# Performance work log

Hardware: AMD Instinct MI355X
Metric: run time of the kernel (lower is better)

## Reference

```python
import jax, jax.numpy as jnp
import numpy as np

N_HEAD, D_K, D_V, D_MODEL = 12, 64, 64, 768
SMOOTH = 1e-06
LN_EPS = 1e-06


def _layer_norm(x, g, b, eps=LN_EPS):
    m = x.mean(-1, keepdims=True)
    v = x.var(-1, keepdims=True)
    return (x - m) / jnp.sqrt(v + eps) * g + b


def setup_inputs() -> dict:
    key = jax.random.key(0)
    ks = jax.random.split(key, 12)
    b, L, R = 4, 1024, 97
    w = lambda k, i, o: jax.random.normal(k, (i, o), jnp.float32) * 0.02
    return {
        'doc_input': jax.random.normal(ks[0], (b, L, D_MODEL), jnp.float32),
        'rel_input': jax.random.normal(ks[1], (b, R, D_MODEL), jnp.float32),
        'mask': jax.random.randint(ks[2], (b, L), 0, 2, jnp.int32),
        'wq_doc': w(ks[3], D_MODEL, N_HEAD * D_K),
        'wk_doc': w(ks[4], D_MODEL, N_HEAD * D_K),
        'wv_doc': w(ks[5], D_MODEL, N_HEAD * D_V),
        'wk_rel': w(ks[6], D_MODEL, N_HEAD * D_K),
        'wv_rel': w(ks[7], D_MODEL, N_HEAD * D_V),
        'fc_doc': w(ks[8], N_HEAD * D_V, D_MODEL),
        'fc_rel': w(ks[9], N_HEAD * D_V, D_MODEL),
        'ln_doc_g': jnp.ones((D_MODEL,), jnp.float32),
        'ln_doc_b': jnp.zeros((D_MODEL,), jnp.float32),
        'ln_rel_g': jnp.ones((D_MODEL,), jnp.float32),
        'ln_rel_b': jnp.zeros((D_MODEL,), jnp.float32),
    }


def _forward(doc_input, rel_input, mask, wq_doc, wk_doc, wv_doc, wk_rel, wv_rel,
             fc_doc, fc_rel, ln_doc_g, ln_doc_b, ln_rel_g, ln_rel_b):
    b, L, _ = doc_input.shape
    R = rel_input.shape[1]
    proj = lambda x, w, d: (x @ w).reshape(x.shape[0], x.shape[1], N_HEAD, d).transpose(0, 2, 1, 3)
    dq = proj(doc_input, wq_doc, D_K)   # [b,h,L,dk]
    dk = proj(doc_input, wk_doc, D_K)
    dv = proj(doc_input, wv_doc, D_V)
    rk = proj(rel_input, wk_rel, D_K)   # [b,h,R,dk]
    rv = proj(rel_input, wv_rel, D_V)

    scale = 1.0 / np.sqrt(D_K).astype(np.float32)
    key_mask = (mask == 0)[:, None, None, :]  # [b,1,1,L]

    # doc-doc attention with relation-summed key fusion
    fused_k = dk + rk.sum(2, keepdims=True)  # broadcast [b,h,1,dk]
    scores = jnp.einsum('bhid,bhjd->bhij', dq, fused_k) * scale + SMOOTH
    scores = jnp.where(key_mask, -1e9, scores)
    alpha_dd = jax.nn.softmax(scores, axis=-1)  # dropout disabled (eval)

    # per-relation cross attention, batched over R (replaces python loop)
    rscores = jnp.einsum('bhrd,bhjd->bhrj', rk, dk) * scale + SMOOTH
    rscores = jnp.where(key_mask, -1e9, rscores)
    alpha_r = jax.nn.softmax(rscores, axis=-1)
    psi_r = jnp.einsum('bhrj,bhjd->bhrd', alpha_r, dv) + rv  # [b,h,R,dv]
    psi_r = psi_r.transpose(0, 2, 1, 3).reshape(b, R, N_HEAD * D_V)
    rel_output = _layer_norm(psi_r @ fc_rel + rel_input, ln_rel_g, ln_rel_b)

    fused_v = dv + rv.sum(2, keepdims=True)
    psi_i = jnp.einsum('bhij,bhjd->bhid', alpha_dd, fused_v)  # [b,h,L,dv]
    psi_i = psi_i.transpose(0, 2, 1, 3).reshape(b, L, N_HEAD * D_V)
    doc_output = _layer_norm(psi_i @ fc_doc + doc_input, ln_doc_g, ln_doc_b)
    return doc_output, rel_output


def reference(doc_input, rel_input, mask, wq_doc, wk_doc, wv_doc, wk_rel, wv_rel,
              fc_doc, fc_rel, ln_doc_g, ln_doc_b, ln_rel_g, ln_rel_b):
    return _forward(doc_input, rel_input, mask, wq_doc, wk_doc, wv_doc, wk_rel,
                    wv_rel, fc_doc, fc_rel, ln_doc_g, ln_doc_b, ln_rel_g, ln_rel_b)
```

## Files before the change

kernel.cpp:

```cpp
#include <hip/hip_runtime.h>

typedef __attribute__((ext_vector_type(8))) short bt8;
typedef __attribute__((ext_vector_type(4))) float f32x4;

__device__ __forceinline__ float bf2f(ushort u) {
    union { unsigned int i; float f; } v; v.i = ((unsigned int)u) << 16; return v.f;
}
__device__ __forceinline__ ushort f2bf(float f) {
    union { float f; unsigned int i; } v; v.f = f;
    unsigned int r = v.i + 0x7fffu + ((v.i >> 16) & 1u);
    return (ushort)(r >> 16);
}

#define GLOAD_LDS16(gp, lp) __builtin_amdgcn_global_load_lds( \
    (const __attribute__((address_space(1))) unsigned int*)(gp), \
    (__attribute__((address_space(3))) unsigned int*)(lp), 16, 0, 0)

__global__ __launch_bounds__(256) void cvt_bf16(const float* __restrict__ in,
                                                ushort* __restrict__ out, int n) {
    int i = blockIdx.x * 256 + threadIdx.x;
    if (i < n) out[i] = f2bf(in[i]);
}

__global__ void transpose_all(const float* __restrict__ p0, const float* __restrict__ p1,
                              const float* __restrict__ p2, const float* __restrict__ p3,
                              const float* __restrict__ p4, const float* __restrict__ p5,
                              const float* __restrict__ p6, ushort* __restrict__ out) {
    __shared__ float t[32][33];
    const float* W;
    switch (blockIdx.z) {
        case 0: W = p0; break; case 1: W = p1; break; case 2: W = p2; break;
        case 3: W = p3; break; case 4: W = p4; break; case 5: W = p5; break;
        default: W = p6; break;
    }
    ushort* WT = out + (size_t)blockIdx.z * 768 * 768;
    int bx = blockIdx.x * 32, by = blockIdx.y * 32;
    int x = threadIdx.x, y0 = threadIdx.y;
    for (int y = y0; y < 32; y += 8)
        t[y][x] = W[(size_t)(by + y) * 768 + bx + x];
    __syncthreads();
    for (int y = y0; y < 32; y += 8)
        WT[(size_t)(bx + y) * 768 + by + x] = f2bf(t[x][y]);
}

template<bool BF16O>
__global__ __launch_bounds__(256) void gemm_gl(
    const ushort* __restrict__ A, const ushort* __restrict__ BT,
    void* __restrict__ Cv, int M, int N, int K)
{
    __shared__ ushort As[128 * 32];
    __shared__ ushort Bs[128 * 32];
    const int tid = threadIdx.x;
    const int wave = tid >> 6, lane = tid & 63;
    const int row0 = blockIdx.x * 128, col0 = blockIdx.y * 128;
    const int wm = (wave >> 1) * 64, wn = (wave & 1) * 64;
    const int lr = lane & 15, lk = (lane >> 4) * 8;
    const int srow = wave * 16 + (lane >> 2);
    const int scol = (lane & 3) * 8;

    f32x4 acc[4][4];
    #pragma unroll
    for (int mi = 0; mi < 4; ++mi)
        #pragma unroll
        for (int ni = 0; ni < 4; ++ni)
            acc[mi][ni] = (f32x4){0.f, 0.f, 0.f, 0.f};

    int ar0 = row0 + srow;       if (ar0 >= M) ar0 = M - 1;
    int ar1 = row0 + 64 + srow;  if (ar1 >= M) ar1 = M - 1;
    const int bc0 = col0 + srow, bc1 = col0 + 64 + srow;

    for (int kt = 0; kt < K; kt += 32) {
        __syncthreads();
        GLOAD_LDS16(A + (size_t)ar0 * K + kt + scol, As + wave * 512);
        GLOAD_LDS16(A + (size_t)ar1 * K + kt + scol, As + 2048 + wave * 512);
        GLOAD_LDS16(BT + (size_t)bc0 * K + kt + scol, Bs + wave * 512);
        GLOAD_LDS16(BT + (size_t)bc1 * K + kt + scol, Bs + 2048 + wave * 512);
        __syncthreads();
        bt8 af[4], bf[4];
        #pragma unroll
        for (int mi = 0; mi < 4; ++mi)
            af[mi] = *(const bt8*)&As[(wm + mi * 16 + lr) * 32 + lk];
        #pragma unroll
        for (int ni = 0; ni < 4; ++ni)
            bf[ni] = *(const bt8*)&Bs[(wn + ni * 16 + lr) * 32 + lk];
        #pragma unroll
        for (int mi = 0; mi < 4; ++mi)
            #pragma unroll
            for (int ni = 0; ni < 4; ++ni)
                acc[mi][ni] = __builtin_amdgcn_mfma_f32_16x16x32_bf16(
                    af[mi], bf[ni], acc[mi][ni], 0, 0, 0);
    }

    #pragma unroll
    for (int mi = 0; mi < 4; ++mi) {
        int orow0 = row0 + wm + mi * 16 + (lane >> 4) * 4;
        #pragma unroll
        for (int ni = 0; ni < 4; ++ni) {
            int ocol = col0 + wn + ni * 16 + lr;
            if (ocol >= N) continue;
            #pragma unroll
            for (int r2 = 0; r2 < 4; ++r2) {
                int orow = orow0 + r2;
                if (orow < M) {
                    if (BF16O)
                        ((ushort*)Cv)[(size_t)orow * N + ocol] = f2bf(acc[mi][ni][r2]);
                    else
                        ((float*)Cv)[(size_t)orow * N + ocol] = acc[mi][ni][r2];
                }
            }
        }
    }
}

__global__ void relsum(const ushort* __restrict__ rkv,
                       float* __restrict__ rks, float* __restrict__ rvs) {
    int b = blockIdx.x;
    int c = blockIdx.y * 256 + threadIdx.x;
    float s1 = 0.f, s2 = 0.f;
    for (int r = 0; r < 97; ++r) {
        const ushort* row = rkv + (size_t)(b * 97 + r) * 1536;
        s1 += bf2f(row[c]);
        s2 += bf2f(row[768 + c]);
    }
    rks[b * 768 + c] = s1;
    rvs[b * 768 + c] = s2;
}

__global__ __launch_bounds__(256) void fusekv(
    const ushort* __restrict__ qkv, const float* __restrict__ rks,
    const float* __restrict__ rvs, ushort* __restrict__ kf, ushort* __restrict__ vf)
{
    int row = blockIdx.x;
    int c = blockIdx.y * 256 + threadIdx.x;
    int b = row >> 10;
    size_t qi = (size_t)row * 2304;
    size_t oi = (size_t)row * 768 + c;
    kf[oi] = f2bf(bf2f(qkv[qi + 768 + c]) + rks[b * 768 + c]);
    vf[oi] = f2bf(bf2f(qkv[qi + 1536 + c]) + rvs[b * 768 + c]);
}

__global__ __launch_bounds__(256) void attn_mfma(
    const ushort* __restrict__ Qp, int qstride, size_t qbstride, int qmax,
    const ushort* __restrict__ Kp, const ushort* __restrict__ Vp,
    int kvstride, size_t kvbstride,
    const int* __restrict__ mask,
    float* __restrict__ Mo, float* __restrict__ Lo, ushort* __restrict__ Oo,
    int nspl, int ntiles, int qrows)
{
    __shared__ ushort Ks[64 * 64];
    __shared__ ushort Vt[64 * 64];
    __shared__ ushort Ps[4][16 * 64];
    __shared__ float  madd[64];

    const int tid = threadIdx.x;
    const int wv = tid >> 6, lane = tid & 63;
    const int lr = lane & 15, lk = (lane >> 4) * 8, rg = lane >> 4;
    const int bh = blockIdx.x, b = bh / 12, h = bh % 12;
    const int qb = blockIdx.y, spl = blockIdx.z;
    const int q0 = qb * 64 + wv * 16;

    const size_t kvbase = (size_t)b * kvbstride + h * 64;
    const size_t qbase  = (size_t)b * qbstride + h * 64;

    bt8 qf[2];
    {
        const int qi = q0 + lr;
        if (qi < qmax) {
            const ushort* qp = Qp + qbase + (size_t)qi * qstride + lk;
            qf[0] = *(const bt8*)qp;
            qf[1] = *(const bt8*)(qp + 32);
        } else {
            #pragma unroll
            for (int j = 0; j < 8; ++j) { qf[0][j] = 0; qf[1][j] = 0; }
        }
    }

    f32x4 acc[4];
    #pragma unroll
    for (int dg = 0; dg < 4; ++dg) acc[dg] = (f32x4){0.f, 0.f, 0.f, 0.f};
    float m_r[4], l_r[4];
    #pragma unroll
    for (int r = 0; r < 4; ++r) { m_r[r] = -3.0e38f; l_r[r] = 0.f; }

    const int key = tid >> 2, c0 = (tid & 3) * 16;
    const int vd = tid & 63, vw = tid >> 6;
    const int swk = (key & 7) << 3;
    const int swv = (vd & 7) << 3;
    const int swl = (lr & 7) << 3;

    for (int t = 0; t < ntiles; ++t) {
        const int k0 = (spl * ntiles + t) * 64;
        __syncthreads();
        {
            const ushort* src = Kp + kvbase + (size_t)(k0 + key) * kvstride + c0;
            int4 a = *(const int4*)src;
            int4 bq = *(const int4*)(src + 8);
            *(int4*)&Ks[key * 64 + (c0 ^ swk)] = a;
            *(int4*)&Ks[key * 64 + ((c0 + 8) ^ swk)] = bq;
        }
        {
            const ushort* vsrc = Vp + kvbase + (size_t)(k0 + vw * 16) * kvstride + vd;
            ushort tv[16];
            #pragma unroll
            for (int j = 0; j < 16; ++j) tv[j] = vsrc[(size_t)j * kvstride];
            const int cc = vw * 16;
            *(int4*)&Vt[vd * 64 + (cc ^ swv)] = *(int4*)tv;
            *(int4*)&Vt[vd * 64 + ((cc + 8) ^ swv)] = *(int4*)(tv + 8);
        }
        if (tid < 64)
            madd[tid] = (mask[b * 1024 + k0 + tid] == 0) ? -1e30f : 0.f;
        __syncthreads();

        f32x4 sf[4];
        #pragma unroll
        for (int kg = 0; kg < 4; ++kg) {
            f32x4 s4 = (f32x4){0.f, 0.f, 0.f, 0.f};
            #pragma unroll
            for (int kk = 0; kk < 2; ++kk) {
                bt8 kf2 = *(const bt8*)&Ks[(kg * 16 + lr) * 64 + ((kk * 32 + lk) ^ swl)];
                s4 = __builtin_amdgcn_mfma_f32_16x16x32_bf16(qf[kk], kf2, s4, 0, 0, 0);
            }
            sf[kg] = s4;
        }

        float pv[4][4];
        #pragma unroll
        for (int r = 0; r < 4; ++r) {
            float sv0 = sf[0][r] * 0.125f + madd[lr];
            float sv1 = sf[1][r] * 0.125f + madd[16 + lr];
            float sv2 = sf[2][r] * 0.125f + madd[32 + lr];
            float sv3 = sf[3][r] * 0.125f + madd[48 + lr];
            float mx = fmaxf(fmaxf(sv0, sv1), fmaxf(sv2, sv3));
            mx = fmaxf(mx, __shfl_xor(mx, 1));
            mx = fmaxf(mx, __shfl_xor(mx, 2));
            mx = fmaxf(mx, __shfl_xor(mx, 4));
            mx = fmaxf(mx, __shfl_xor(mx, 8));
            float mn = fmaxf(m_r[r], mx);
            float corr = __expf(m_r[r] - mn);
            m_r[r] = mn;
            float p0 = __expf(sv0 - mn), p1 = __expf(sv1 - mn);
            float p2 = __expf(sv2 - mn), p3 = __expf(sv3 - mn);
            pv[0][r] = p0; pv[1][r] = p1; pv[2][r] = p2; pv[3][r] = p3;
            float ps = (p0 + p1) + (p2 + p3);
            ps += __shfl_xor(ps, 1);
            ps += __shfl_xor(ps, 2);
            ps += __shfl_xor(ps, 4);
            ps += __shfl_xor(ps, 8);
            l_r[r] = l_r[r] * corr + ps;
            #pragma unroll
            for (int dg = 0; dg < 4; ++dg) acc[dg][r] *= corr;
        }

        #pragma unroll
        for (int kg = 0; kg < 4; ++kg)
            #pragma unroll
            for (int r = 0; r < 4; ++r) {
                int rowq = rg * 4 + r;
                Ps[wv][rowq * 64 + ((kg * 16 + lr) ^ ((rowq & 7) << 3))] = f2bf(pv[kg][r]);
            }

        #pragma unroll
        for (int kk = 0; kk < 2; ++kk) {
            bt8 pa = *(const bt8*)&Ps[wv][lr * 64 + ((kk * 32 + lk) ^ swl)];
            #pragma unroll
            for (int dg = 0; dg < 4; ++dg) {
                bt8 vf2 = *(const bt8*)&Vt[(dg * 16 + lr) * 64 + ((kk * 32 + lk) ^ swl)];
                acc[dg] = __builtin_amdgcn_mfma_f32_16x16x32_bf16(pa, vf2, acc[dg], 0, 0, 0);
            }
        }
    }

    if (lr == 0) {
        #pragma unroll
        for (int r = 0; r < 4; ++r) {
            int qi = q0 + rg * 4 + r;
            int prow = (bh * nspl + spl) * qrows + qi;
            Mo[prow] = m_r[r];
            Lo[prow] = l_r[r];
        }
    }
    #pragma unroll
    for (int r = 0; r < 4; ++r) {
        int qi = q0 + rg * 4 + r;
        size_t orow = ((size_t)(bh * nspl + spl) * qrows + qi) * 64;
        #pragma unroll
        for (int dg = 0; dg < 4; ++dg)
            Oo[orow + dg * 16 + lr] = f2bf(acc[dg][r]);
    }
}

__global__ __launch_bounds__(64) void attn_merge(
    const float* __restrict__ Mo, const float* __restrict__ Lo, const ushort* __restrict__ Oo,
    const ushort* __restrict__ resid, size_t rbstride, int rstride,
    ushort* __restrict__ psi,
    int nspl, int qrows, int qmax, int out_rows)
{
    const int tid = threadIdx.x, bh = blockIdx.x, qb = blockIdx.y;
    const int b = bh / 12, h = bh % 12;
    const int qi = qb * 64 + tid;
    if (qi >= qmax) return;
    const int pb = bh * nspl;

    float M = -3.0e38f;
    for (int s = 0; s < nspl; ++s)
        M = fmaxf(M, Mo[(pb + s) * qrows + qi]);
    float L = 0.f, O[64];
    #pragma unroll
    for (int d = 0; d < 64; ++d) O[d] = 0.f;
    for (int s = 0; s < nspl; ++s) {
        int pr = (pb + s) * qrows + qi;
        float f = __expf(Mo[pr] - M);
        L += Lo[pr] * f;
        const uint* op = (const uint*)(Oo + (size_t)pr * 64);
        #pragma unroll
        for (int d2 = 0; d2 < 32; ++d2) {
            uint u = op[d2];
            O[2*d2]   += f * bf2f((ushort)(u & 0xffffu));
            O[2*d2+1] += f * bf2f((ushort)(u >> 16));
        }
    }
    const float rl = 1.f / L;
    const size_t ob = ((size_t)b * out_rows + qi) * 768 + h * 64;
    if (resid) {
        const ushort* rp = resid + (size_t)b * rbstride + (size_t)qi * rstride + h * 64;
        #pragma unroll
        for (int d = 0; d < 64; ++d)
            psi[ob + d] = f2bf(O[d] * rl + bf2f(rp[d]));
    } else {
        #pragma unroll
        for (int d = 0; d < 64; ++d)
            psi[ob + d] = f2bf(O[d] * rl);
    }
}

__global__ __launch_bounds__(256) void ln_ker(
    const float* __restrict__ gin, const float* __restrict__ resid,
    const float* __restrict__ g, const float* __restrict__ bta,
    float* __restrict__ out)
{
    const int row = blockIdx.x, tid = threadIdx.x;
    const size_t rb = (size_t)row * 768;
    float x[3], s = 0.f, s2 = 0.f;
    #pragma unroll
    for (int k2 = 0; k2 < 3; ++k2) {
        int c = k2 * 256 + tid;
        float v = gin[rb + c] + resid[rb + c];
        x[k2] = v; s += v; s2 += v * v;
    }
    #pragma unroll
    for (int off = 32; off > 0; off >>= 1) {
        s  += __shfl_down(s, off);
        s2 += __shfl_down(s2, off);
    }
    __shared__ float red[10];
    const int wv = tid >> 6;
    if ((tid & 63) == 0) { red[wv] = s; red[4 + wv] = s2; }
    __syncthreads();
    if (tid == 0) {
        float ts = red[0] + red[1] + red[2] + red[3];
        float t2 = red[4] + red[5] + red[6] + red[7];
        float mean = ts * (1.f / 768.f);
        float var = t2 * (1.f / 768.f) - mean * mean;
        red[8] = mean;
        red[9] = rsqrtf(fmaxf(var, 0.f) + 1e-6f);
    }
    __syncthreads();
    const float mean = red[8], rstd = red[9];
    #pragma unroll
    for (int k2 = 0; k2 < 3; ++k2) {
        int c = k2 * 256 + tid;
        out[rb + c] = (x[k2] - mean) * rstd * g[c] + bta[c];
    }
}

extern "C" void kernel_launch(void* const* d_in, const int* in_sizes, int n_in,
                              void* d_out, int out_size, void* d_ws, size_t ws_size,
                              hipStream_t stream) {
    const float* doc  = (const float*)d_in[0];
    const float* rel  = (const float*)d_in[1];
    const int*   mask = (const int*)d_in[2];
    const float* ln_dg = (const float*)d_in[10];
    const float* ln_db = (const float*)d_in[11];
    const float* ln_rg = (const float*)d_in[12];
    const float* ln_rb = (const float*)d_in[13];

    char* ws = (char*)d_ws;
    size_t off = 0;
    ushort* wtall = (ushort*)(ws + off); off += (size_t)7 * 768 * 768 * 2;
    ushort* wtqkv = wtall;
    ushort* wt34  = wtall + (size_t)3 * 768 * 768;
    ushort* wt5   = wtall + (size_t)5 * 768 * 768;
    ushort* wt6   = wtall + (size_t)6 * 768 * 768;
    ushort* doc_bf = (ushort*)(ws + off); off += (size_t)4096 * 768 * 2;
    ushort* rel_bf = (ushort*)(ws + off); off += (size_t)388 * 768 * 2;
    ushort* qkv_bf = (ushort*)(ws + off); off += (size_t)4096 * 2304 * 2;
    ushort* rkv_bf = (ushort*)(ws + off); off += (size_t)388 * 1536 * 2;
    float*  rks = (float*)(ws + off); off += (size_t)4 * 768 * 4;
    float*  rvs = (float*)(ws + off); off += (size_t)4 * 768 * 4;
    ushort* kf_bf = (ushort*)(ws + off); off += (size_t)4096 * 768 * 2;
    ushort* vf_bf = (ushort*)(ws + off); off += (size_t)4096 * 768 * 2;
    ushort* psi_i = (ushort*)(ws + off); off += (size_t)4096 * 768 * 2;
    ushort* psi_r = (ushort*)(ws + off); off += (size_t)388 * 768 * 2;
    float*  Mo = (float*)(ws + off);  off += (size_t)48 * 2 * 1024 * 4;
    float*  Lo = (float*)(ws + off);  off += (size_t)48 * 2 * 1024 * 4;
    ushort* Oo = (ushort*)(ws + off); off += (size_t)48 * 2 * 1024 * 64 * 2;
    float*  gdoc = (float*)(ws + off); off += (size_t)4096 * 768 * 4;
    float*  grel = (float*)(ws + off); off += (size_t)388 * 768 * 4;

    float* out_doc = (float*)d_out;
    float* out_rel = out_doc + (size_t)4096 * 768;

    cvt_bf16<<<dim3((4096 * 768 + 255) / 256), 256, 0, stream>>>(doc, doc_bf, 4096 * 768);
    cvt_bf16<<<dim3((388 * 768 + 255) / 256), 256, 0, stream>>>(rel, rel_bf, 388 * 768);
    transpose_all<<<dim3(24, 24, 7), dim3(32, 8), 0, stream>>>(
        (const float*)d_in[3], (const float*)d_in[4], (const float*)d_in[5],
        (const float*)d_in[6], (const float*)d_in[7], (const float*)d_in[8],
        (const float*)d_in[9], wtall);

    gemm_gl<true><<<dim3(32, 18), 256, 0, stream>>>(doc_bf, wtqkv, qkv_bf, 4096, 2304, 768);
    gemm_gl<true><<<dim3(4, 12),  256, 0, stream>>>(rel_bf, wt34, rkv_bf, 388, 1536, 768);

    relsum<<<dim3(4, 3), 256, 0, stream>>>(rkv_bf, rks, rvs);
    fusekv<<<dim3(4096, 3), 256, 0, stream>>>(qkv_bf, rks, rvs, kf_bf, vf_bf);

    attn_mfma<<<dim3(48, 2, 8), 256, 0, stream>>>(
        rkv_bf, 1536, (size_t)97 * 1536, 97,
        qkv_bf + 768, qkv_bf + 1536, 2304, (size_t)1024 * 2304,
        mask, Mo, Lo, Oo, 8, 2, 128);
    attn_merge<<<dim3(48, 2), 64, 0, stream>>>(
        Mo, Lo, Oo, rkv_bf + 768, (size_t)97 * 1536, 1536, psi_r, 8, 128, 97, 97);

    attn_mfma<<<dim3(48, 16, 2), 256, 0, stream>>>(
        qkv_bf, 2304, (size_t)1024 * 2304, 1024,
        kf_bf, vf_bf, 768, (size_t)1024 * 768,
        mask, Mo, Lo, Oo, 2, 8, 1024);
    attn_merge<<<dim3(48, 16), 64, 0, stream>>>(
        Mo, Lo, Oo, (const ushort*)nullptr, 0, 0, psi_i, 2, 1024, 1024, 1024);

    gemm_gl<false><<<dim3(32, 6), 256, 0, stream>>>(psi_i, wt5, gdoc, 4096, 768, 768);
    gemm_gl<false><<<dim3(4, 6),  256, 0, stream>>>(psi_r, wt6, grel, 388, 768, 768);

    ln_ker<<<4096, 256, 0, stream>>>(gdoc, doc, ln_dg, ln_db, out_doc);
    ln_ker<<<388,  256, 0, stream>>>(grel, rel, ln_rg, ln_rb, out_rel);
}
```

Measured before the change: 216.3 us.

## Widen attention query tile, add lazy-rescale exp2 softmax, small-tile GEMMs, fused convert

The attention kernel now gives each wave 32 query rows instead of 16, so each block covers 128 queries and the K/V tiles loaded into shared memory are reused across twice as many rows. The softmax switches to exp2 with the scale folded into one constant, and it rescales the running max only when the max grows by more than a threshold. A new 64x64-tile GEMM replaces the larger-tile GEMM for the small and output projections to launch more blocks. The two fp32-to-bf16 conversions are merged into one launch. The costs are more registers per thread in attention and possible numeric drift from the deferred rescale.

```diff
diff --git a/kernel.cpp b/kernel.cpp
--- a/kernel.cpp
+++ b/kernel.cpp
@@ -16,10 +16,12 @@
     (const __attribute__((address_space(1))) unsigned int*)(gp), \
     (__attribute__((address_space(3))) unsigned int*)(lp), 16, 0, 0)
 
-__global__ __launch_bounds__(256) void cvt_bf16(const float* __restrict__ in,
-                                                ushort* __restrict__ out, int n) {
+__global__ __launch_bounds__(256) void cvt_two(
+    const float* __restrict__ a, const float* __restrict__ b,
+    ushort* __restrict__ oa, ushort* __restrict__ ob, int n1, int n2) {
     int i = blockIdx.x * 256 + threadIdx.x;
-    if (i < n) out[i] = f2bf(in[i]);
+    if (i < n1) oa[i] = f2bf(a[i]);
+    else if (i < n1 + n2) ob[i - n1] = f2bf(b[i - n1]);
 }
 
 __global__ void transpose_all(const float* __restrict__ p0, const float* __restrict__ p1,
@@ -112,6 +114,72 @@
     }
 }
 
+template<bool BF16O>
+__global__ __launch_bounds__(256) void gemm64(
+    const ushort* __restrict__ A, const ushort* __restrict__ BT,
+    void* __restrict__ Cv, int M, int N, int K)
+{
+    __shared__ ushort As[64 * 32];
+    __shared__ ushort Bs[64 * 32];
+    const int tid = threadIdx.x;
+    const int wave = tid >> 6, lane = tid & 63;
+    const int row0 = blockIdx.x * 64, col0 = blockIdx.y * 64;
+    const int wm = (wave >> 1) * 32, wn = (wave & 1) * 32;
+    const int lr = lane & 15, lk = (lane >> 4) * 8;
+    const int srow = tid >> 2;
+    const int scol = (tid & 3) * 8;
+
+    f32x4 acc[2][2];
+    #pragma unroll
+    for (int mi = 0; mi < 2; ++mi)
+        #pragma unroll
+        for (int ni = 0; ni < 2; ++ni)
+            acc[mi][ni] = (f32x4){0.f, 0.f, 0.f, 0.f};
+
+    int ar = row0 + srow; if (ar >= M) ar = M - 1;
+    const int bc = col0 + srow;
+
+    for (int kt = 0; kt < K; kt += 32) {
+        __syncthreads();
+        GLOAD_LDS16(A + (size_t)ar * K + kt + scol, As + wave * 512);
+        GLOAD_LDS16(BT + (size_t)bc * K + kt + scol, Bs + wave * 512);
+        __syncthreads();
+        bt8 af[2], bf[2];
+        #pragma unroll
+        for (int mi = 0; mi < 2; ++mi)
+            af[mi] = *(const bt8*)&As[(wm + mi * 16 + lr) * 32 + lk];
+        #pragma unroll
+        for (int ni = 0; ni < 2; ++ni)
+            bf[ni] = *(const bt8*)&Bs[(wn + ni * 16 + lr) * 32 + lk];
+        #pragma unroll
+        for (int mi = 0; mi < 2; ++mi)
+            #pragma unroll
+            for (int ni = 0; ni < 2; ++ni)
+                acc[mi][ni] = __builtin_amdgcn_mfma_f32_16x16x32_bf16(
+                    af[mi], bf[ni], acc[mi][ni], 0, 0, 0);
+    }
+
+    #pragma unroll
+    for (int mi = 0; mi < 2; ++mi) {
+        int orow0 = row0 + wm + mi * 16 + (lane >> 4) * 4;
+        #pragma unroll
+        for (int ni = 0; ni < 2; ++ni) {
+            int ocol = col0 + wn + ni * 16 + lr;
+            if (ocol >= N) continue;
+            #pragma unroll
+            for (int r2 = 0; r2 < 4; ++r2) {
+                int orow = orow0 + r2;
+                if (orow < M) {
+                    if (BF16O)
+                        ((ushort*)Cv)[(size_t)orow * N + ocol] = f2bf(acc[mi][ni][r2]);
+                    else
+                        ((float*)Cv)[(size_t)orow * N + ocol] = acc[mi][ni][r2];
+                }
+            }
+        }
+    }
+}
+
 __global__ void relsum(const ushort* __restrict__ rkv,
                        float* __restrict__ rks, float* __restrict__ rvs) {
     int b = blockIdx.x;
@@ -139,6 +207,9 @@
     vf[oi] = f2bf(bf2f(qkv[qi + 1536 + c]) + rvs[b * 768 + c]);
 }
 
+#define SC2 0.18033688011112042f
+#define THR2 10.0f
+
 __global__ __launch_bounds__(256) void attn_mfma(
     const ushort* __restrict__ Qp, int qstride, size_t qbstride, int qmax,
     const ushort* __restrict__ Kp, const ushort* __restrict__ Vp,
@@ -149,7 +220,7 @@
 {
     __shared__ ushort Ks[64 * 64];
     __shared__ ushort Vt[64 * 64];
-    __shared__ ushort Ps[4][16 * 64];
+    __shared__ ushort Ps[4][32 * 64];
     __shared__ float  madd[64];
 
     const int tid = threadIdx.x;
@@ -157,30 +228,33 @@
     const int lr = lane & 15, lk = (lane >> 4) * 8, rg = lane >> 4;
     const int bh = blockIdx.x, b = bh / 12, h = bh % 12;
     const int qb = blockIdx.y, spl = blockIdx.z;
-    const int q0 = qb * 64 + wv * 16;
+    const int q0 = qb * 128 + wv * 32;
 
     const size_t kvbase = (size_t)b * kvbstride + h * 64;
     const size_t qbase  = (size_t)b * qbstride + h * 64;
 
-    bt8 qf[2];
-    {
-        const int qi = q0 + lr;
+    bt8 qf[2][2];
+    #pragma unroll
+    for (int qh = 0; qh < 2; ++qh) {
+        const int qi = q0 + qh * 16 + lr;
         if (qi < qmax) {
             const ushort* qp = Qp + qbase + (size_t)qi * qstride + lk;
-            qf[0] = *(const bt8*)qp;
-            qf[1] = *(const bt8*)(qp + 32);
+            qf[qh][0] = *(const bt8*)qp;
+            qf[qh][1] = *(const bt8*)(qp + 32);
         } else {
             #pragma unroll
-            for (int j = 0; j < 8; ++j) { qf[0][j] = 0; qf[1][j] = 0; }
-        }
-    }
-
-    f32x4 acc[4];
-    #pragma unroll
-    for (int dg = 0; dg < 4; ++dg) acc[dg] = (f32x4){0.f, 0.f, 0.f, 0.f};
-    float m_r[4], l_r[4];
-    #pragma unroll
-    for (int r = 0; r < 4; ++r) { m_r[r] = -3.0e38f; l_r[r] = 0.f; }
+            for (int j = 0; j < 8; ++j) { qf[qh][0][j] = 0; qf[qh][1][j] = 0; }
+        }
+    }
+
+    f32x4 acc[2][4];
+    #pragma unroll
+    for (int qh = 0; qh < 2; ++qh)
+        #pragma unroll
+        for (int dg = 0; dg < 4; ++dg) acc[qh][dg] = (f32x4){0.f, 0.f, 0.f, 0.f};
+    float m_r[8], l_r[8];
+    #pragma unroll
+    for (int r = 0; r < 8; ++r) { m_r[r] = -3.0e38f; l_r[r] = 0.f; }
 
     const int key = tid >> 2, c0 = (tid & 3) * 16;
     const int vd = tid & 63, vw = tid >> 6;
@@ -211,82 +285,93 @@
             madd[tid] = (mask[b * 1024 + k0 + tid] == 0) ? -1e30f : 0.f;
         __syncthreads();
 
-        f32x4 sf[4];
-        #pragma unroll
-        for (int kg = 0; kg < 4; ++kg) {
-            f32x4 s4 = (f32x4){0.f, 0.f, 0.f, 0.f};
+        #pragma unroll
+        for (int qh = 0; qh < 2; ++qh) {
+            f32x4 sf[4];
+            #pragma unroll
+            for (int kg = 0; kg < 4; ++kg) {
+                f32x4 s4 = (f32x4){0.f, 0.f, 0.f, 0.f};
+                #pragma unroll
+                for (int kk = 0; kk < 2; ++kk) {
+                    bt8 kf2 = *(const bt8*)&Ks[(kg * 16 + lr) * 64 + ((kk * 32 + lk) ^ swl)];
+                    s4 = __builtin_amdgcn_mfma_f32_16x16x32_bf16(qf[qh][kk], kf2, s4, 0, 0, 0);
+                }
+                sf[kg] = s4;
+            }
+
+            #pragma unroll
+            for (int r = 0; r < 4; ++r) {
+                const int ri = qh * 4 + r;
+                float sv0 = sf[0][r] * SC2 + madd[lr];
+                float sv1 = sf[1][r] * SC2 + madd[16 + lr];
+                float sv2 = sf[2][r] * SC2 + madd[32 + lr];
+                float sv3 = sf[3][r] * SC2 + madd[48 + lr];
+                float mx = fmaxf(fmaxf(sv0, sv1), fmaxf(sv2, sv3));
+                mx = fmaxf(mx, __shfl_xor(mx, 1));
+                mx = fmaxf(mx, __shfl_xor(mx, 2));
+                mx = fmaxf(mx, __shfl_xor(mx, 4));
+                mx = fmaxf(mx, __shfl_xor(mx, 8));
+                float m_old = m_r[ri];
+                if (mx > m_old + THR2) {
+                    float corr = exp2f(m_old - mx);
+                    m_r[ri] = mx;
+                    l_r[ri] *= corr;
+                    #pragma unroll
+                    for (int dg = 0; dg < 4; ++dg) acc[qh][dg][r] *= corr;
+                }
+                const float mn = m_r[ri];
+                float p0 = exp2f(sv0 - mn), p1 = exp2f(sv1 - mn);
+                float p2 = exp2f(sv2 - mn), p3 = exp2f(sv3 - mn);
+                float ps = (p0 + p1) + (p2 + p3);
+                ps += __shfl_xor(ps, 1);
+                ps += __shfl_xor(ps, 2);
+                ps += __shfl_xor(ps, 4);
+                ps += __shfl_xor(ps, 8);
+                l_r[ri] += ps;
+                const int rowq = qh * 16 + rg * 4 + r;
+                const int swp = (rowq & 7) << 3;
+                Ps[wv][rowq * 64 + ((0 * 16 + lr) ^ swp)] = f2bf(p0);
+                Ps[wv][rowq * 64 + ((1 * 16 + lr) ^ swp)] = f2bf(p1);
+                Ps[wv][rowq * 64 + ((2 * 16 + lr) ^ swp)] = f2bf(p2);
+                Ps[wv][rowq * 64 + ((3 * 16 + lr) ^ swp)] = f2bf(p3);
+            }
+        }
+
+        #pragma unroll
+        for (int qh = 0; qh < 2; ++qh) {
             #pragma unroll
             for (int kk = 0; kk < 2; ++kk) {
-                bt8 kf2 = *(const bt8*)&Ks[(kg * 16 + lr) * 64 + ((kk * 32 + lk) ^ swl)];
-                s4 = __builtin_amdgcn_mfma_f32_16x16x32_bf16(qf[kk], kf2, s4, 0, 0, 0);
+                bt8 pa = *(const bt8*)&Ps[wv][(qh * 16 + lr) * 64 + ((kk * 32 + lk) ^ swl)];
+                #pragma unroll
+                for (int dg = 0; dg < 4; ++dg) {
+                    bt8 vf2 = *(const bt8*)&Vt[(dg * 16 + lr) * 64 + ((kk * 32 + lk) ^ swl)];
+                    acc[qh][dg] = __builtin_amdgcn_mfma_f32_16x16x32_bf16(pa, vf2, acc[qh][dg], 0, 0, 0);
+                }
             }
-            sf[kg] = s4;
-        }
-
-        float pv[4][4];
+        }
+    }
+
+    if (lr == 0) {
+        #pragma unroll
+        for (int qh = 0; qh < 2; ++qh)
+            #pragma unroll
+            for (int r = 0; r < 4; ++r) {
+                int qi = q0 + qh * 16 + rg * 4 + r;
+                int prow = (bh * nspl + spl) * qrows + qi;
+                Mo[prow] = m_r[qh * 4 + r];
+                Lo[prow] = l_r[qh * 4 + r];
+            }
+    }
+    #pragma unroll
+    for (int qh = 0; qh < 2; ++qh)
         #pragma unroll
         for (int r = 0; r < 4; ++r) {
-            float sv0 = sf[0][r] * 0.125f + madd[lr];
-            float sv1 = sf[1][r] * 0.125f + madd[16 + lr];
-            float sv2 = sf[2][r] * 0.125f + madd[32 + lr];
-            float sv3 = sf[3][r] * 0.125f + madd[48 + lr];
-            float mx = fmaxf(fmaxf(sv0, sv1), fmaxf(sv2, sv3));
-            mx = fmaxf(mx, __shfl_xor(mx, 1));
-            mx = fmaxf(mx, __shfl_xor(mx, 2));
-            mx = fmaxf(mx, __shfl_xor(mx, 4));
-            mx = fmaxf(mx, __shfl_xor(mx, 8));
-            float mn = fmaxf(m_r[r], mx);
-            float corr = __expf(m_r[r] - mn);
-            m_r[r] = mn;
-            float p0 = __expf(sv0 - mn), p1 = __expf(sv1 - mn);
-            float p2 = __expf(sv2 - mn), p3 = __expf(sv3 - mn);
-            pv[0][r] = p0; pv[1][r] = p1; pv[2][r] = p2; pv[3][r] = p3;
-            float ps = (p0 + p1) + (p2 + p3);
-            ps += __shfl_xor(ps, 1);
-            ps += __shfl_xor(ps, 2);
-            ps += __shfl_xor(ps, 4);
-            ps += __shfl_xor(ps, 8);
-            l_r[r] = l_r[r] * corr + ps;
-            #pragma unroll
-            for (int dg = 0; dg < 4; ++dg) acc[dg][r] *= corr;
-        }
-
-        #pragma unroll
-        for (int kg = 0; kg < 4; ++kg)
-            #pragma unroll
-            for (int r = 0; r < 4; ++r) {
-                int rowq = rg * 4 + r;
-                Ps[wv][rowq * 64 + ((kg * 16 + lr) ^ ((rowq & 7) << 3))] = f2bf(pv[kg][r]);
-            }
-
-        #pragma unroll
-        for (int kk = 0; kk < 2; ++kk) {
-            bt8 pa = *(const bt8*)&Ps[wv][lr * 64 + ((kk * 32 + lk) ^ swl)];
-            #pragma unroll
-            for (int dg = 0; dg < 4; ++dg) {
-                bt8 vf2 = *(const bt8*)&Vt[(dg * 16 + lr) * 64 + ((kk * 32 + lk) ^ swl)];
-                acc[dg] = __builtin_amdgcn_mfma_f32_16x16x32_bf16(pa, vf2, acc[dg], 0, 0, 0);
-            }
-        }
-    }
-
-    if (lr == 0) {
-        #pragma unroll
-        for (int r = 0; r < 4; ++r) {
-            int qi = q0 + rg * 4 + r;
-            int prow = (bh * nspl + spl) * qrows + qi;
-            Mo[prow] = m_r[r];
-            Lo[prow] = l_r[r];
-        }
-    }
-    #pragma unroll
-    for (int r = 0; r < 4; ++r) {
-        int qi = q0 + rg * 4 + r;
-        size_t orow = ((size_t)(bh * nspl + spl) * qrows + qi) * 64;
-        #pragma unroll
-        for (int dg = 0; dg < 4; ++dg)
-            Oo[orow + dg * 16 + lr] = f2bf(acc[dg][r]);
-    }
+            int qi = q0 + qh * 16 + rg * 4 + r;
+            size_t orow = ((size_t)(bh * nspl + spl) * qrows + qi) * 64;
+            #pragma unroll
+            for (int dg = 0; dg < 4; ++dg)
+                Oo[orow + dg * 16 + lr] = f2bf(acc[qh][dg][r]);
+        }
 }
 
 __global__ __launch_bounds__(64) void attn_merge(
@@ -309,7 +394,7 @@
     for (int d = 0; d < 64; ++d) O[d] = 0.f;
     for (int s = 0; s < nspl; ++s) {
         int pr = (pb + s) * qrows + qi;
-        float f = __expf(Mo[pr] - M);
+        float f = exp2f(Mo[pr] - M);
         L += Lo[pr] * f;
         const uint* op = (const uint*)(Oo + (size_t)pr * 64);
         #pragma unroll
@@ -410,35 +495,35 @@
     float* out_doc = (float*)d_out;
     float* out_rel = out_doc + (size_t)4096 * 768;
 
-    cvt_bf16<<<dim3((4096 * 768 + 255) / 256), 256, 0, stream>>>(doc, doc_bf, 4096 * 768);
-    cvt_bf16<<<dim3((388 * 768 + 255) / 256), 256, 0, stream>>>(rel, rel_bf, 388 * 768);
+    const int n1 = 4096 * 768, n2 = 388 * 768;
+    cvt_two<<<dim3((n1 + n2 + 255) / 256), 256, 0, stream>>>(doc, rel, doc_bf, rel_bf, n1, n2);
     transpose_all<<<dim3(24, 24, 7), dim3(32, 8), 0, stream>>>(
         (const float*)d_in[3], (const float*)d_in[4], (const float*)d_in[5],
         (const float*)d_in[6], (const float*)d_in[7], (const float*)d_in[8],
         (const float*)d_in[9], wtall);
 
     gemm_gl<true><<<dim3(32, 18), 256, 0, stream>>>(doc_bf, wtqkv, qkv_bf, 4096, 2304, 768);
-    gemm_gl<true><<<dim3(4, 12),  256, 0, stream>>>(rel_bf, wt34, rkv_bf, 388, 1536, 768);
+    gemm64<true><<<dim3(7, 24),  256, 0, stream>>>(rel_bf, wt34, rkv_bf, 388, 1536, 768);
 
     relsum<<<dim3(4, 3), 256, 0, stream>>>(rkv_bf, rks, rvs);
     fusekv<<<dim3(4096, 3), 256, 0, stream>>>(qkv_bf, rks, rvs, kf_bf, vf_bf);
 
-    attn_mfma<<<dim3(48, 2, 8), 256, 0, stream>>>(
+    attn_mfma<<<dim3(48, 1, 8), 256, 0, stream>>>(
         rkv_bf, 1536, (size_t)97 * 1536, 97,
         qkv_bf + 768, qkv_bf + 1536, 2304, (size_t)1024 * 2304,
         mask, Mo, Lo, Oo, 8, 2, 128);
     attn_merge<<<dim3(48, 2), 64, 0, stream>>>(
         Mo, Lo, Oo, rkv_bf + 768, (size_t)97 * 1536, 1536, psi_r, 8, 128, 97, 97);
 
-    attn_mfma<<<dim3(48, 16, 2), 256, 0, stream>>>(
+    attn_mfma<<<dim3(48, 8, 2), 256, 0, stream>>>(
         qkv_bf, 2304, (size_t)1024 * 2304, 1024,
         kf_bf, vf_bf, 768, (size_t)1024 * 768,
         mask, Mo, Lo, Oo, 2, 8, 1024);
     attn_merge<<<dim3(48, 16), 64, 0, stream>>>(
         Mo, Lo, Oo, (const ushort*)nullptr, 0, 0, psi_i, 2, 1024, 1024, 1024);
 
-    gemm_gl<false><<<dim3(32, 6), 256, 0, stream>>>(psi_i, wt5, gdoc, 4096, 768, 768);
-    gemm_gl<false><<<dim3(4, 6),  256, 0, stream>>>(psi_r, wt6, grel, 388, 768, 768);
+    gemm64<false><<<dim3(64, 12), 256, 0, stream>>>(psi_i, wt5, gdoc, 4096, 768, 768);
+    gemm64<false><<<dim3(7, 12),  256, 0, stream>>>(psi_r, wt6, grel, 388, 768, 768);
 
     ln_ker<<<4096, 256, 0, stream>>>(gdoc, doc, ln_dg, ln_db, out_doc);
     ln_ker<<<388,  256, 0, stream>>>(grel, rel, ln_rg, ln_rb, out_rel);
```

Result: no change. 216.4 us (+0.1%).
